# Kernel tuning notes

Hardware: AMD Instinct MI355X
Metric: run time of the kernel (lower is better)

The kernel has to match this reference:

```python
import jax, jax.numpy as jnp
import numpy as np

NUM_HEADS = 8
EPS = 1e-12  # matches torch F.normalize default eps


def setup_inputs() -> dict:
    key = jax.random.key(0)
    k1, k2 = jax.random.split(key)
    x = jax.random.normal(k1, (8, 384, 128, 128), dtype=jnp.float32)
    # 1x1 conv weight [out=3*dim, in=dim]
    w_qkv = jax.random.normal(k2, (1152, 384), dtype=jnp.float32) * (1.0 / np.sqrt(384))
    return {"x": x, "w_qkv": w_qkv}


def _l2norm(t):
    # torch F.normalize(dim=-1): x / max(||x||2, eps)
    n = jnp.sqrt(jnp.sum(t * t, axis=-1, keepdims=True))
    return t / jnp.maximum(n, EPS)


def reference(x, w_qkv):
    B, C, H, W = x.shape
    hw = H * W
    head_c = C // NUM_HEADS
    # 1x1 conv == channel matmul
    qkv = jnp.einsum('bchw,oc->bohw', x, w_qkv)  # [B, 3C, H, W]
    q, k, v = jnp.split(qkv, 3, axis=1)
    def rs(t):
        return t.reshape(B, NUM_HEADS, head_c, hw)
    q, k, v = rs(q), rs(k), rs(v)
    q = _l2norm(q)
    k = _l2norm(k)
    scale = jnp.sqrt(jnp.float32(hw))
    attn = jnp.einsum('bhcn,bhdn->bhcd', q, k) / scale  # small CxC per head
    attn = jax.nn.softmax(attn, axis=-1)
    out = jnp.einsum('bhcd,bhdn->bhcn', attn, v)
    return out.reshape(B, C, H, W)
```

## Files before the change

kernel.cpp:

```cpp
#include <hip/hip_runtime.h>

typedef short short8 __attribute__((ext_vector_type(8)));
typedef __bf16 bf16x8 __attribute__((ext_vector_type(8)));
typedef float f32x4 __attribute__((ext_vector_type(4)));
typedef int i32x4 __attribute__((ext_vector_type(4)));

typedef const __attribute__((address_space(1))) void* gas_p;
typedef __attribute__((address_space(3))) void* las_p;

static __device__ __forceinline__ unsigned short f2bf(float f) {
  unsigned u = __builtin_bit_cast(unsigned, f);
  u += 0x7fffu + ((u >> 16) & 1u);
  return (unsigned short)(u >> 16);
}
static __device__ __forceinline__ float bf2f(unsigned short h) {
  unsigned u = ((unsigned)h) << 16;
  return __builtin_bit_cast(float, u);
}

#define MFMA16(a, b, c) __builtin_amdgcn_mfma_f32_16x16x32_bf16( \
    __builtin_bit_cast(bf16x8, a), __builtin_bit_cast(bf16x8, b), (c), 0, 0, 0)

__global__ __launch_bounds__(64) void k0_wfrag(const float* __restrict__ w,
                                               unsigned short* __restrict__ wfrag) {
  int bx = blockIdx.x;
  int m16 = bx / 12, kb = bx % 12;
  int lane = threadIdx.x;
  int i = lane & 15, g = lane >> 4;
  int o = m16 * 16 + i;
  int k = kb * 32 + g * 8;
  const float* src = w + (size_t)o * 384 + k;
  f32x4 f0 = *(const f32x4*)(src);
  f32x4 f1 = *(const f32x4*)(src + 4);
  short8 v;
#pragma unroll
  for (int j = 0; j < 4; ++j) { v[j] = (short)f2bf(f0[j]); v[4 + j] = (short)f2bf(f1[j]); }
  *(short8*)(wfrag + ((size_t)(m16 * 12 + kb) * 64 + lane) * 8) = v;
}

__global__ __launch_bounds__(256) void kx_transpose(const float* __restrict__ x,
                                                    unsigned short* __restrict__ xt,
                                                    int bbase) {
  __shared__ unsigned T[64 * 32];
  int n0 = blockIdx.x * 64, c0 = blockIdx.y * 64;
  int bl = blockIdx.z;
  int bg = bbase + bl;
  int t = threadIdx.x;
  int cl2 = t >> 6, nl = t & 63;
  const float* xb = x + ((size_t)bg * 384 + c0) * 16384 + n0 + nl;
#pragma unroll
  for (int u = 0; u < 8; ++u) {
    int cb = cl2 * 2 + u * 8;
    float f0 = xb[(size_t)cb * 16384];
    float f1 = xb[(size_t)(cb + 1) * 16384];
    unsigned p = (unsigned)f2bf(f0) | ((unsigned)f2bf(f1) << 16);
    int cp = cb >> 1;
    T[nl * 32 + (cp ^ (nl & 31))] = p;
  }
  __syncthreads();
  int nl2 = t >> 2, cg = t & 3;
  unsigned vals[8];
#pragma unroll
  for (int j = 0; j < 8; ++j)
    vals[j] = T[nl2 * 32 + ((cg * 8 + j) ^ (nl2 & 31))];
  unsigned short* dst = xt + ((size_t)bl * 16384 + n0 + nl2) * 384 + c0 + cg * 16;
  *(i32x4*)(dst)     = (i32x4){(int)vals[0], (int)vals[1], (int)vals[2], (int)vals[3]};
  *(i32x4*)(dst + 8) = (i32x4){(int)vals[4], (int)vals[5], (int)vals[6], (int)vals[7]};
}

__global__ __launch_bounds__(256, 4) void k1_qkv(const unsigned short* __restrict__ xt,
                                                 const unsigned short* __restrict__ wfrag,
                                                 unsigned short* __restrict__ qkv,
                                                 float* __restrict__ norms2,
                                                 int bbase, int nb) {
  __shared__ union {
    unsigned short Bt[2][128 * 32];
    unsigned short Cl[128 * 136];
  } sm;

  int flat = blockIdx.x;
  int b_l = flat % nb;
  int rem = flat / nb;
  int m = rem % 9, ntile = rem / 9;
  int o0 = m * 128, n0 = ntile * 128;
  int bg = bbase + b_l;
  int t = threadIdx.x;
  int wave = t >> 6, lane = t & 63;
  int i = lane & 15, g = lane >> 4;
  int mh = wave >> 1, nh = wave & 1;

  const unsigned short* xrow = xt + ((size_t)b_l * 16384 + n0 + (t >> 2)) * 384 + (t & 3) * 8;

  f32x4 acc[4][4];
#pragma unroll
  for (int a = 0; a < 4; ++a)
#pragma unroll
    for (int c = 0; c < 4; ++c) acc[a][c] = (f32x4){0.f, 0.f, 0.f, 0.f};

#define STAGE(buf, kb)                                                          \
  do {                                                                          \
    const unsigned short* s0 = xrow + (kb) * 32;                                \
    unsigned short* d0 = &sm.Bt[0][0] + (buf) * 4096 + t * 8;                   \
    __builtin_amdgcn_global_load_lds((gas_p)s0, (las_p)d0, 16, 0, 0);           \
    __builtin_amdgcn_global_load_lds((gas_p)(s0 + (size_t)64 * 384),            \
                                     (las_p)(d0 + 2048), 16, 0, 0);             \
  } while (0)

  STAGE(0, 0);
  for (int kb = 0; kb < 12; ++kb) {
    __syncthreads();
    if (kb < 11) STAGE((kb + 1) & 1, kb + 1);
    short8 aF[4];
#pragma unroll
    for (int mt = 0; mt < 4; ++mt)
      aF[mt] = *(const short8*)(wfrag + ((size_t)((m * 8 + mh * 4 + mt) * 12 + kb) * 64 + lane) * 8);
    const unsigned short* bbaseL = &sm.Bt[kb & 1][(nh * 64) * 32 + g * 8];
#pragma unroll
    for (int nt = 0; nt < 4; ++nt) {
      short8 bF = *(const short8*)(bbaseL + (nt * 16 + i) * 32);
#pragma unroll
      for (int mt = 0; mt < 4; ++mt) acc[mt][nt] = MFMA16(aF[mt], bF, acc[mt][nt]);
    }
  }
#undef STAGE

  __syncthreads();

#pragma unroll
  for (int mt = 0; mt < 4; ++mt)
#pragma unroll
    for (int nt = 0; nt < 4; ++nt)
#pragma unroll
      for (int rr = 0; rr < 4; ++rr)
        sm.Cl[(mh * 64 + mt * 16 + 4 * g + rr) * 136 + nh * 64 + nt * 16 + i] =
            f2bf(acc[mt][nt][rr]);
  __syncthreads();

  size_t obase = ((size_t)bg * 1152 + o0) * 16384 + n0;
  int srow = t >> 4, scol = (t & 15) * 8;
#pragma unroll
  for (int u = 0; u < 8; ++u) {
    int row = u * 16 + srow;
    short8 vv = *(const short8*)&sm.Cl[row * 136 + scol];
    *(short8*)(qkv + obase + (size_t)row * 16384 + scol) = vv;
  }

  if (o0 < 768) {
    int row = t >> 1, half = t & 1;
    const unsigned short* p = &sm.Cl[row * 136 + half * 64];
    float s = 0.f;
#pragma unroll
    for (int u = 0; u < 8; ++u) {
      short8 vv = *(const short8*)(p + u * 8);
#pragma unroll
      for (int e = 0; e < 8; ++e) {
        float f = bf2f((unsigned short)vv[e]);
        s += f * f;
      }
    }
    s += __shfl_xor(s, 1, 64);
    if (half == 0) atomicAdd(&norms2[bg * 768 + o0 + row], s);
  }
}

__global__ __launch_bounds__(256) void k2_gram(const unsigned short* __restrict__ qkv,
                                               float* __restrict__ G) {
  __shared__ float Gl[48 * 48];
  int bh = blockIdx.x >> 4, chunk = blockIdx.x & 15;
  int b = bh >> 3, hi = bh & 7;
  int t = threadIdx.x, wave = t >> 6, lane = t & 63;
  int i = lane & 15, g = lane >> 4;
  for (int u = t; u < 2304; u += 256) Gl[u] = 0.f;
  __syncthreads();

  const unsigned short* qbase = qkv + ((size_t)b * 1152 + hi * 48) * 16384;
  const unsigned short* kbase = qbase + (size_t)384 * 16384;
  int pos0 = chunk * 1024 + wave * 256;

  f32x4 acc[3][3];
#pragma unroll
  for (int a = 0; a < 3; ++a)
#pragma unroll
    for (int c = 0; c < 3; ++c) acc[a][c] = (f32x4){0.f, 0.f, 0.f, 0.f};

  for (int ks = 0; ks < 8; ++ks) {
    int kp = pos0 + ks * 32 + g * 8;
    short8 aF[3], bF[3];
#pragma unroll
    for (int mt = 0; mt < 3; ++mt)
      aF[mt] = *(const short8*)(qbase + (size_t)(mt * 16 + i) * 16384 + kp);
#pragma unroll
    for (int nt = 0; nt < 3; ++nt)
      bF[nt] = *(const short8*)(kbase + (size_t)(nt * 16 + i) * 16384 + kp);
#pragma unroll
    for (int mt = 0; mt < 3; ++mt)
#pragma unroll
      for (int nt = 0; nt < 3; ++nt) acc[mt][nt] = MFMA16(aF[mt], bF[nt], acc[mt][nt]);
  }
#pragma unroll
  for (int mt = 0; mt < 3; ++mt)
#pragma unroll
    for (int nt = 0; nt < 3; ++nt)
#pragma unroll
      for (int rr = 0; rr < 4; ++rr)
        atomicAdd(&Gl[(mt * 16 + 4 * g + rr) * 48 + nt * 16 + i], acc[mt][nt][rr]);
  __syncthreads();
  float* Gg = G + (size_t)bh * 2304;
  for (int u = t; u < 2304; u += 256) atomicAdd(&Gg[u], Gl[u]);
}

__global__ __launch_bounds__(64) void k2b_softmax(const float* __restrict__ G,
                                                  const float* __restrict__ norms2,
                                                  float* __restrict__ attn) {
  int bh = blockIdx.x;
  int b = bh >> 3, hi = bh & 7;
  int c = threadIdx.x;
  if (c >= 48) return;
  const float* Gg = G + (size_t)bh * 2304 + c * 48;
  const float* nq = norms2 + b * 768 + hi * 48;
  const float* nk = nq + 384;
  float dq = fmaxf(sqrtf(nq[c]), 1e-12f);
  float l[48];
  float m = -1e30f;
#pragma unroll
  for (int d = 0; d < 48; ++d) {
    float dk = fmaxf(sqrtf(nk[d]), 1e-12f);
    l[d] = Gg[d] / (dq * dk * 128.0f);
    m = fmaxf(m, l[d]);
  }
  float s = 0.f;
#pragma unroll
  for (int d = 0; d < 48; ++d) {
    l[d] = expf(l[d] - m);
    s += l[d];
  }
  float inv = 1.0f / s;
  float* A = attn + (size_t)bh * 2304 + c * 48;
#pragma unroll
  for (int d = 0; d < 48; ++d) A[d] = l[d] * inv;
}

__global__ __launch_bounds__(256) void k3_out(const unsigned short* __restrict__ qkv,
                                              const float* __restrict__ attn,
                                              float* __restrict__ out) {
  __shared__ unsigned short Vt[256 * 72];
  int nchunk = blockIdx.x, bh = blockIdx.y;
  int b = bh >> 3, hi = bh & 7;
  int n0 = nchunk * 256;
  int t = threadIdx.x, wave = t >> 6, lane = t & 63;
  int i = lane & 15, g = lane >> 4;

  const unsigned short* vbase = qkv + ((size_t)b * 1152 + 768 + hi * 48) * 16384 + n0 + t;
  unsigned short* vr = &Vt[t * 72];
#pragma unroll
  for (int dp = 0; dp < 24; ++dp) {
    unsigned a0 = vbase[(size_t)(2 * dp) * 16384];
    unsigned a1 = vbase[(size_t)(2 * dp + 1) * 16384];
    *(unsigned*)(vr + 2 * dp) = a0 | (a1 << 16);
  }
  *(i32x4*)(vr + 48) = (i32x4){0, 0, 0, 0};
  *(i32x4*)(vr + 56) = (i32x4){0, 0, 0, 0};

  const float* Ab = attn + (size_t)bh * 2304;
  short8 aF[3][2];
#pragma unroll
  for (int mt = 0; mt < 3; ++mt) {
    int row = mt * 16 + i;
    f32x4 f0 = *(const f32x4*)(Ab + row * 48 + 8 * g);
    f32x4 f1 = *(const f32x4*)(Ab + row * 48 + 8 * g + 4);
    short8 a0;
#pragma unroll
    for (int j = 0; j < 4; ++j) { a0[j] = (short)f2bf(f0[j]); a0[4 + j] = (short)f2bf(f1[j]); }
    aF[mt][0] = a0;
    short8 a1v = (short8){0, 0, 0, 0, 0, 0, 0, 0};
    if (g < 2) {
      f32x4 h0 = *(const f32x4*)(Ab + row * 48 + 32 + 8 * g);
      f32x4 h1 = *(const f32x4*)(Ab + row * 48 + 32 + 8 * g + 4);
#pragma unroll
      for (int j = 0; j < 4; ++j) { a1v[j] = (short)f2bf(h0[j]); a1v[4 + j] = (short)f2bf(h1[j]); }
    }
    aF[mt][1] = a1v;
  }
  __syncthreads();

  f32x4 acc[3][4];
#pragma unroll
  for (int a = 0; a < 3; ++a)
#pragma unroll
    for (int c = 0; c < 4; ++c) acc[a][c] = (f32x4){0.f, 0.f, 0.f, 0.f};

  int nb = wave * 64;
#pragma unroll
  for (int nt = 0; nt < 4; ++nt) {
    const unsigned short* vp = &Vt[(size_t)(nb + nt * 16 + i) * 72 + 8 * g];
    short8 b0 = *(const short8*)vp;
    short8 b1 = *(const short8*)(vp + 32);
#pragma unroll
    for (int mt = 0; mt < 3; ++mt) {
      acc[mt][nt] = MFMA16(aF[mt][0], b0, acc[mt][nt]);
      acc[mt][nt] = MFMA16(aF[mt][1], b1, acc[mt][nt]);
    }
  }

  float* ob = out + ((size_t)b * 384 + hi * 48) * 16384 + n0 + nb;
#pragma unroll
  for (int mt = 0; mt < 3; ++mt)
#pragma unroll
    for (int nt = 0; nt < 4; ++nt)
#pragma unroll
      for (int rr = 0; rr < 4; ++rr)
        ob[(size_t)(mt * 16 + 4 * g + rr) * 16384 + nt * 16 + i] = acc[mt][nt][rr];
}

extern "C" void kernel_launch(void* const* d_in, const int* in_sizes, int n_in,
                              void* d_out, int out_size, void* d_ws, size_t ws_size,
                              hipStream_t stream) {
  const float* x = (const float*)d_in[0];
  const float* w = (const float*)d_in[1];
  float* out = (float*)d_out;
  char* ws = (char*)d_ws;

  unsigned short* qkv   = (unsigned short*)(ws);
  unsigned short* wfrag = (unsigned short*)(ws + 301989888LL);
  float* norms2         = (float*)(ws + 302874624LL);
  float* G              = (float*)(ws + 302899200LL);
  float* attn           = (float*)(ws + 303489024LL);
  unsigned short* xtb   = (unsigned short*)(ws + 304078848LL);

  const size_t FULL_NEED = 304078848LL + 100663296LL;

  hipMemsetAsync(ws + 302874624LL, 0, 24576 + 589824, stream);
  k0_wfrag<<<864, 64, 0, stream>>>(w, wfrag);

  if (ws_size >= FULL_NEED) {
    kx_transpose<<<dim3(256, 6, 8), 256, 0, stream>>>(x, xtb, 0);
    k1_qkv<<<9216, 256, 0, stream>>>(xtb, wfrag, qkv, norms2, 0, 8);
  } else {
    for (int b = 0; b < 8; ++b) {
      kx_transpose<<<dim3(256, 6, 1), 256, 0, stream>>>(x, xtb, b);
      k1_qkv<<<1152, 256, 0, stream>>>(xtb, wfrag, qkv, norms2, b, 1);
    }
  }

  k2_gram<<<1024, 256, 0, stream>>>(qkv, G);
  k2b_softmax<<<64, 64, 0, stream>>>(G, norms2, attn);
  k3_out<<<dim3(64, 64), 256, 0, stream>>>(qkv, attn, out);
}
```

Before: 390.1 us.

## Swizzle LDS staging in QKV GEMM and stage Gram inputs via LDS

```diff
diff --git a/kernel.cpp b/kernel.cpp
--- a/kernel.cpp
+++ b/kernel.cpp
@@ -89,7 +89,12 @@
   int i = lane & 15, g = lane >> 4;
   int mh = wave >> 1, nh = wave & 1;
 
-  const unsigned short* xrow = xt + ((size_t)b_l * 16384 + n0 + (t >> 2)) * 384 + (t & 3) * 8;
+  int r = t >> 2, blk = t & 3;
+  int srcblk = blk ^ (r & 3);
+  const unsigned short* xrow =
+      xt + ((size_t)b_l * 16384 + n0 + r) * 384 + srcblk * 8;
+
+  const unsigned short* wbase = wfrag + ((size_t)(m * 8 + mh * 4) * 12 * 64 + lane) * 8;
 
   f32x4 acc[4][4];
 #pragma unroll
@@ -106,20 +111,27 @@
                                      (las_p)(d0 + 2048), 16, 0, 0);             \
   } while (0)
 
+  short8 aF[4];
+#pragma unroll
+  for (int mt = 0; mt < 4; ++mt)
+    aF[mt] = *(const short8*)(wbase + (size_t)(mt * 12) * 512);
   STAGE(0, 0);
+
   for (int kb = 0; kb < 12; ++kb) {
     __syncthreads();
     if (kb < 11) STAGE((kb + 1) & 1, kb + 1);
-    short8 aF[4];
-#pragma unroll
-    for (int mt = 0; mt < 4; ++mt)
-      aF[mt] = *(const short8*)(wfrag + ((size_t)((m * 8 + mh * 4 + mt) * 12 + kb) * 64 + lane) * 8);
-    const unsigned short* bbaseL = &sm.Bt[kb & 1][(nh * 64) * 32 + g * 8];
+    const unsigned short* bb = &sm.Bt[kb & 1][0];
+    int swz = (g ^ (i & 3)) * 8;
 #pragma unroll
     for (int nt = 0; nt < 4; ++nt) {
-      short8 bF = *(const short8*)(bbaseL + (nt * 16 + i) * 32);
+      short8 bF = *(const short8*)(bb + (nh * 64 + nt * 16 + i) * 32 + swz);
 #pragma unroll
       for (int mt = 0; mt < 4; ++mt) acc[mt][nt] = MFMA16(aF[mt], bF, acc[mt][nt]);
+    }
+    if (kb < 11) {
+#pragma unroll
+      for (int mt = 0; mt < 4; ++mt)
+        aF[mt] = *(const short8*)(wbase + (size_t)(mt * 12 + kb + 1) * 512);
     }
   }
 #undef STAGE
@@ -165,17 +177,36 @@
 
 __global__ __launch_bounds__(256) void k2_gram(const unsigned short* __restrict__ qkv,
                                                float* __restrict__ G) {
+  __shared__ unsigned short Bt[2][96 * 128];
   __shared__ float Gl[48 * 48];
   int bh = blockIdx.x >> 4, chunk = blockIdx.x & 15;
   int b = bh >> 3, hi = bh & 7;
   int t = threadIdx.x, wave = t >> 6, lane = t & 63;
   int i = lane & 15, g = lane >> 4;
+
   for (int u = t; u < 2304; u += 256) Gl[u] = 0.f;
-  __syncthreads();
-
-  const unsigned short* qbase = qkv + ((size_t)b * 1152 + hi * 48) * 16384;
-  const unsigned short* kbase = qbase + (size_t)384 * 16384;
-  int pos0 = chunk * 1024 + wave * 256;
+
+  const unsigned short* qrow = qkv + ((size_t)b * 1152 + hi * 48) * 16384;
+  const unsigned short* krow = qrow + (size_t)384 * 16384;
+  int P = chunk * 1024;
+
+  int srow = t >> 4;
+  int sblk = (t & 15) ^ (srow & 7);
+
+#define STAGE2(buf, tt)                                                         \
+  do {                                                                          \
+    int p0 = P + (tt) * 128 + sblk * 8;                                         \
+    unsigned short* d0 = &Bt[buf][0] + t * 8;                                   \
+    _Pragma("unroll")                                                           \
+    for (int e = 0; e < 3; ++e) {                                               \
+      __builtin_amdgcn_global_load_lds(                                         \
+          (gas_p)(qrow + (size_t)(e * 16 + srow) * 16384 + p0),                 \
+          (las_p)(d0 + e * 2048), 16, 0, 0);                                    \
+      __builtin_amdgcn_global_load_lds(                                         \
+          (gas_p)(krow + (size_t)(e * 16 + srow) * 16384 + p0),                 \
+          (las_p)(d0 + (e + 3) * 2048), 16, 0, 0);                              \
+    }                                                                           \
+  } while (0)
 
   f32x4 acc[3][3];
 #pragma unroll
@@ -183,20 +214,28 @@
 #pragma unroll
     for (int c = 0; c < 3; ++c) acc[a][c] = (f32x4){0.f, 0.f, 0.f, 0.f};
 
-  for (int ks = 0; ks < 8; ++ks) {
-    int kp = pos0 + ks * 32 + g * 8;
+  STAGE2(0, 0);
+  int ksg = wave * 4 + g;
+  for (int tt = 0; tt < 8; ++tt) {
+    __syncthreads();
+    if (tt < 7) STAGE2((tt + 1) & 1, tt + 1);
+    const unsigned short* bb = &Bt[tt & 1][0];
+    int d = (ksg ^ (i & 7)) * 8;
     short8 aF[3], bF[3];
 #pragma unroll
     for (int mt = 0; mt < 3; ++mt)
-      aF[mt] = *(const short8*)(qbase + (size_t)(mt * 16 + i) * 16384 + kp);
+      aF[mt] = *(const short8*)(bb + (mt * 16 + i) * 128 + d);
 #pragma unroll
     for (int nt = 0; nt < 3; ++nt)
-      bF[nt] = *(const short8*)(kbase + (size_t)(nt * 16 + i) * 16384 + kp);
+      bF[nt] = *(const short8*)(bb + (48 + nt * 16 + i) * 128 + d);
 #pragma unroll
     for (int mt = 0; mt < 3; ++mt)
 #pragma unroll
       for (int nt = 0; nt < 3; ++nt) acc[mt][nt] = MFMA16(aF[mt], bF[nt], acc[mt][nt]);
   }
+#undef STAGE2
+
+  __syncthreads();
 #pragma unroll
   for (int mt = 0; mt < 3; ++mt)
 #pragma unroll
```

Result: no change. 392.2 us (+0.5%).

## Fuse Q/K projection with Gram matrix and norm accumulation per head tile

Applied to the files above, without the earlier changes.

```diff
diff --git a/kernel.cpp b/kernel.cpp
--- a/kernel.cpp
+++ b/kernel.cpp
@@ -68,20 +68,154 @@
   *(i32x4*)(dst + 8) = (i32x4){(int)vals[4], (int)vals[5], (int)vals[6], (int)vals[7]};
 }
 
-__global__ __launch_bounds__(256, 4) void k1_qkv(const unsigned short* __restrict__ xt,
-                                                 const unsigned short* __restrict__ wfrag,
-                                                 unsigned short* __restrict__ qkv,
-                                                 float* __restrict__ norms2,
-                                                 int bbase, int nb) {
+
+__global__ __launch_bounds__(256, 4) void k1_head(const unsigned short* __restrict__ xt,
+                                                  const unsigned short* __restrict__ wfrag,
+                                                  float* __restrict__ G,
+                                                  float* __restrict__ norms2,
+                                                  int bbase, int nb) {
   __shared__ union {
-    unsigned short Bt[2][128 * 32];
-    unsigned short Cl[128 * 136];
+    unsigned short Bt[2][128 * 64];
+    struct { unsigned short Cl[96 * 136]; float Gl[48 * 48]; } ep;
   } sm;
 
   int flat = blockIdx.x;
   int b_l = flat % nb;
   int rem = flat / nb;
-  int m = rem % 9, ntile = rem / 9;
+  int h = rem & 7, ntile = rem >> 3;
+  int n0 = ntile * 128;
+  int bg = bbase + b_l;
+  int t = threadIdx.x;
+  int wave = t >> 6, lane = t & 63;
+  int i = lane & 15, g = lane >> 4;
+
+  int nloc = t >> 3;
+  int sblk = (t & 7) ^ (nloc & 7);
+  const unsigned short* xrow =
+      xt + ((size_t)b_l * 16384 + n0 + nloc) * 384 + sblk * 8;
+
+#define STG(buf, step)                                                        \
+  do {                                                                        \
+    _Pragma("unroll")                                                         \
+    for (int e = 0; e < 4; ++e)                                               \
+      __builtin_amdgcn_global_load_lds(                                       \
+          (gas_p)(xrow + (size_t)(e * 32) * 384 + (step) * 64),               \
+          (las_p)(&sm.Bt[buf][(e * 256 + t) * 8]), 16, 0, 0);                 \
+  } while (0)
+
+  f32x4 acc[6][2];
+#pragma unroll
+  for (int a = 0; a < 6; ++a)
+#pragma unroll
+    for (int c = 0; c < 2; ++c) acc[a][c] = (f32x4){0.f, 0.f, 0.f, 0.f};
+
+  STG(0, 0);
+  for (int st = 0; st < 6; ++st) {
+    __syncthreads();
+    if (st < 5) STG((st + 1) & 1, st + 1);
+    const unsigned short* bb = &sm.Bt[st & 1][0];
+#pragma unroll
+    for (int kk = 0; kk < 2; ++kk) {
+      int kbi = st * 2 + kk;
+      short8 aF[6];
+#pragma unroll
+      for (int mf = 0; mf < 6; ++mf) {
+        int o16 = (mf < 3) ? (h * 3 + mf) : (24 + h * 3 + (mf - 3));
+        aF[mf] = *(const short8*)(wfrag + ((size_t)(o16 * 12 + kbi) * 64 + lane) * 8);
+      }
+#pragma unroll
+      for (int nt = 0; nt < 2; ++nt) {
+        int n = wave * 32 + nt * 16 + i;
+        short8 bF = *(const short8*)(bb + n * 64 + ((kk * 4 + g) ^ (n & 7)) * 8);
+#pragma unroll
+        for (int mf = 0; mf < 6; ++mf) acc[mf][nt] = MFMA16(aF[mf], bF, acc[mf][nt]);
+      }
+    }
+  }
+
+  __syncthreads();
+
+#pragma unroll
+  for (int mf = 0; mf < 6; ++mf)
+#pragma unroll
+    for (int nt = 0; nt < 2; ++nt)
+#pragma unroll
+      for (int rr = 0; rr < 4; ++rr)
+        sm.ep.Cl[(mf * 16 + 4 * g + rr) * 136 + wave * 32 + nt * 16 + i] =
+            f2bf(acc[mf][nt][rr]);
+  for (int u = t; u < 2304; u += 256) sm.ep.Gl[u] = 0.f;
+  __syncthreads();
+
+  f32x4 gacc[3][3];
+#pragma unroll
+  for (int a = 0; a < 3; ++a)
+#pragma unroll
+    for (int c = 0; c < 3; ++c) gacc[a][c] = (f32x4){0.f, 0.f, 0.f, 0.f};
+  {
+    int kp = wave * 32 + g * 8;
+    short8 aG[3], bG[3];
+#pragma unroll
+    for (int mt = 0; mt < 3; ++mt)
+      aG[mt] = *(const short8*)(&sm.ep.Cl[(mt * 16 + i) * 136 + kp]);
+#pragma unroll
+    for (int nt = 0; nt < 3; ++nt)
+      bG[nt] = *(const short8*)(&sm.ep.Cl[(48 + nt * 16 + i) * 136 + kp]);
+#pragma unroll
+    for (int mt = 0; mt < 3; ++mt)
+#pragma unroll
+      for (int nt = 0; nt < 3; ++nt) gacc[mt][nt] = MFMA16(aG[mt], bG[nt], gacc[mt][nt]);
+  }
+
+  {
+    int row = t >> 1, half = t & 1;
+    float s = 0.f;
+    if (row < 96) {
+      const unsigned short* p = &sm.ep.Cl[row * 136 + half * 64];
+#pragma unroll
+      for (int u = 0; u < 8; ++u) {
+        short8 vv = *(const short8*)(p + u * 8);
+#pragma unroll
+        for (int e = 0; e < 8; ++e) {
+          float f = bf2f((unsigned short)vv[e]);
+          s += f * f;
+        }
+      }
+    }
+    s += __shfl_xor(s, 1, 64);
+    if (row < 96 && half == 0) {
+      int idx = (row < 48) ? (bg * 768 + h * 48 + row)
+                           : (bg * 768 + 384 + h * 48 + (row - 48));
+      atomicAdd(&norms2[idx], s);
+    }
+  }
+
+#pragma unroll
+  for (int mt = 0; mt < 3; ++mt)
+#pragma unroll
+    for (int nt = 0; nt < 3; ++nt)
+#pragma unroll
+      for (int rr = 0; rr < 4; ++rr)
+        atomicAdd(&sm.ep.Gl[(mt * 16 + 4 * g + rr) * 48 + nt * 16 + i],
+                  gacc[mt][nt][rr]);
+  __syncthreads();
+  float* Gg = G + (size_t)(bg * 8 + h) * 2304;
+  for (int u = t; u < 2304; u += 256) atomicAdd(&Gg[u], sm.ep.Gl[u]);
+#undef STG
+}
+
+__global__ __launch_bounds__(256, 4) void k1_v(const unsigned short* __restrict__ xt,
+                                               const unsigned short* __restrict__ wfrag,
+                                               unsigned short* __restrict__ qkv,
+                                               int bbase, int nb) {
+  __shared__ union {
+    unsigned short Bt[2][128 * 64];
+    unsigned short Cl[128 * 136];
+  } sm;
+
+  int flat = blockIdx.x;
+  int b_l = flat % nb;
+  int rem = flat / nb;
+  int m = 6 + rem % 3, ntile = rem / 3;
   int o0 = m * 128, n0 = ntile * 128;
   int bg = bbase + b_l;
   int t = threadIdx.x;
@@ -89,7 +223,19 @@
   int i = lane & 15, g = lane >> 4;
   int mh = wave >> 1, nh = wave & 1;
 
-  const unsigned short* xrow = xt + ((size_t)b_l * 16384 + n0 + (t >> 2)) * 384 + (t & 3) * 8;
+  int nloc = t >> 3;
+  int sblk = (t & 7) ^ (nloc & 7);
+  const unsigned short* xrow =
+      xt + ((size_t)b_l * 16384 + n0 + nloc) * 384 + sblk * 8;
+
+#define STG(buf, step)                                                        \
+  do {                                                                        \
+    _Pragma("unroll")                                                         \
+    for (int e = 0; e < 4; ++e)                                               \
+      __builtin_amdgcn_global_load_lds(                                       \
+          (gas_p)(xrow + (size_t)(e * 32) * 384 + (step) * 64),               \
+          (las_p)(&sm.Bt[buf][(e * 256 + t) * 8]), 16, 0, 0);                 \
+  } while (0)
 
   f32x4 acc[4][4];
 #pragma unroll
@@ -97,32 +243,30 @@
 #pragma unroll
     for (int c = 0; c < 4; ++c) acc[a][c] = (f32x4){0.f, 0.f, 0.f, 0.f};
 
-#define STAGE(buf, kb)                                                          \
-  do {                                                                          \
-    const unsigned short* s0 = xrow + (kb) * 32;                                \
-    unsigned short* d0 = &sm.Bt[0][0] + (buf) * 4096 + t * 8;                   \
-    __builtin_amdgcn_global_load_lds((gas_p)s0, (las_p)d0, 16, 0, 0);           \
-    __builtin_amdgcn_global_load_lds((gas_p)(s0 + (size_t)64 * 384),            \
-                                     (las_p)(d0 + 2048), 16, 0, 0);             \
-  } while (0)
-
-  STAGE(0, 0);
-  for (int kb = 0; kb < 12; ++kb) {
+  STG(0, 0);
+  for (int st = 0; st < 6; ++st) {
     __syncthreads();
-    if (kb < 11) STAGE((kb + 1) & 1, kb + 1);
-    short8 aF[4];
-#pragma unroll
-    for (int mt = 0; mt < 4; ++mt)
-      aF[mt] = *(const short8*)(wfrag + ((size_t)((m * 8 + mh * 4 + mt) * 12 + kb) * 64 + lane) * 8);
-    const unsigned short* bbaseL = &sm.Bt[kb & 1][(nh * 64) * 32 + g * 8];
-#pragma unroll
-    for (int nt = 0; nt < 4; ++nt) {
-      short8 bF = *(const short8*)(bbaseL + (nt * 16 + i) * 32);
-#pragma unroll
-      for (int mt = 0; mt < 4; ++mt) acc[mt][nt] = MFMA16(aF[mt], bF, acc[mt][nt]);
-    }
-  }
-#undef STAGE
+    if (st < 5) STG((st + 1) & 1, st + 1);
+    const unsigned short* bb = &sm.Bt[st & 1][0];
+#pragma unroll
+    for (int kk = 0; kk < 2; ++kk) {
+      int kbi = st * 2 + kk;
+      short8 aF[4];
+#pragma unroll
+      for (int mt = 0; mt < 4; ++mt) {
+        int o16 = m * 8 + mh * 4 + mt;
+        aF[mt] = *(const short8*)(wfrag + ((size_t)(o16 * 12 + kbi) * 64 + lane) * 8);
+      }
+#pragma unroll
+      for (int nt = 0; nt < 4; ++nt) {
+        int n = nh * 64 + nt * 16 + i;
+        short8 bF = *(const short8*)(bb + n * 64 + ((kk * 4 + g) ^ (n & 7)) * 8);
+#pragma unroll
+        for (int mt = 0; mt < 4; ++mt) acc[mt][nt] = MFMA16(aF[mt], bF, acc[mt][nt]);
+      }
+    }
+  }
+#undef STG
 
   __syncthreads();
 
@@ -144,69 +288,6 @@
     short8 vv = *(const short8*)&sm.Cl[row * 136 + scol];
     *(short8*)(qkv + obase + (size_t)row * 16384 + scol) = vv;
   }
-
-  if (o0 < 768) {
-    int row = t >> 1, half = t & 1;
-    const unsigned short* p = &sm.Cl[row * 136 + half * 64];
-    float s = 0.f;
-#pragma unroll
-    for (int u = 0; u < 8; ++u) {
-      short8 vv = *(const short8*)(p + u * 8);
-#pragma unroll
-      for (int e = 0; e < 8; ++e) {
-        float f = bf2f((unsigned short)vv[e]);
-        s += f * f;
-      }
-    }
-    s += __shfl_xor(s, 1, 64);
-    if (half == 0) atomicAdd(&norms2[bg * 768 + o0 + row], s);
-  }
-}
-
-__global__ __launch_bounds__(256) void k2_gram(const unsigned short* __restrict__ qkv,
-                                               float* __restrict__ G) {
-  __shared__ float Gl[48 * 48];
-  int bh = blockIdx.x >> 4, chunk = blockIdx.x & 15;
-  int b = bh >> 3, hi = bh & 7;
-  int t = threadIdx.x, wave = t >> 6, lane = t & 63;
-  int i = lane & 15, g = lane >> 4;
-  for (int u = t; u < 2304; u += 256) Gl[u] = 0.f;
-  __syncthreads();
-
-  const unsigned short* qbase = qkv + ((size_t)b * 1152 + hi * 48) * 16384;
-  const unsigned short* kbase = qbase + (size_t)384 * 16384;
-  int pos0 = chunk * 1024 + wave * 256;
-
-  f32x4 acc[3][3];
-#pragma unroll
-  for (int a = 0; a < 3; ++a)
-#pragma unroll
-    for (int c = 0; c < 3; ++c) acc[a][c] = (f32x4){0.f, 0.f, 0.f, 0.f};
-
-  for (int ks = 0; ks < 8; ++ks) {
-    int kp = pos0 + ks * 32 + g * 8;
-    short8 aF[3], bF[3];
-#pragma unroll
-    for (int mt = 0; mt < 3; ++mt)
-      aF[mt] = *(const short8*)(qbase + (size_t)(mt * 16 + i) * 16384 + kp);
-#pragma unroll
-    for (int nt = 0; nt < 3; ++nt)
-      bF[nt] = *(const short8*)(kbase + (size_t)(nt * 16 + i) * 16384 + kp);
-#pragma unroll
-    for (int mt = 0; mt < 3; ++mt)
-#pragma unroll
-      for (int nt = 0; nt < 3; ++nt) acc[mt][nt] = MFMA16(aF[mt], bF[nt], acc[mt][nt]);
-  }
-#pragma unroll
-  for (int mt = 0; mt < 3; ++mt)
-#pragma unroll
-    for (int nt = 0; nt < 3; ++nt)
-#pragma unroll
-      for (int rr = 0; rr < 4; ++rr)
-        atomicAdd(&Gl[(mt * 16 + 4 * g + rr) * 48 + nt * 16 + i], acc[mt][nt][rr]);
-  __syncthreads();
-  float* Gg = G + (size_t)bh * 2304;
-  for (int u = t; u < 2304; u += 256) atomicAdd(&Gg[u], Gl[u]);
 }
 
 __global__ __launch_bounds__(64) void k2b_softmax(const float* __restrict__ G,
@@ -334,15 +415,16 @@
 
   if (ws_size >= FULL_NEED) {
     kx_transpose<<<dim3(256, 6, 8), 256, 0, stream>>>(x, xtb, 0);
-    k1_qkv<<<9216, 256, 0, stream>>>(xtb, wfrag, qkv, norms2, 0, 8);
+    k1_head<<<8192, 256, 0, stream>>>(xtb, wfrag, G, norms2, 0, 8);
+    k1_v<<<3072, 256, 0, stream>>>(xtb, wfrag, qkv, 0, 8);
   } else {
     for (int b = 0; b < 8; ++b) {
       kx_transpose<<<dim3(256, 6, 1), 256, 0, stream>>>(x, xtb, b);
-      k1_qkv<<<1152, 256, 0, stream>>>(xtb, wfrag, qkv, norms2, b, 1);
-    }
-  }
-
-  k2_gram<<<1024, 256, 0, stream>>>(qkv, G);
+      k1_head<<<1024, 256, 0, stream>>>(xtb, wfrag, G, norms2, b, 1);
+      k1_v<<<384, 256, 0, stream>>>(xtb, wfrag, qkv, b, 1);
+    }
+  }
+
   k2b_softmax<<<64, 64, 0, stream>>>(G, norms2, attn);
   k3_out<<<dim3(64, 64), 256, 0, stream>>>(qkv, attn, out);
 }
```

Result: slower. 653.6 us (+67.5%).
